# Kernel optimization log

Hardware: AMD Instinct MI355X
Metric: run time of the kernel (lower is better)

Reference implementation:

```python
import jax, jax.numpy as jnp
import numpy as np

B, N, E = 4, 10000, 160000
IN, OUT, H, ED = 64, 128, 2, 1
SLOPE = 0.2  # GATv2Conv default negative_slope


def _seg_softmax(logits, seg, n):
    # logits: [Ef, H]; softmax over edges sharing the same dst node, per head
    m = jax.ops.segment_max(logits, seg, num_segments=n)
    e = jnp.exp(logits - m[seg])
    d = jax.ops.segment_sum(e, seg, num_segments=n)
    return e / d[seg]


def setup_inputs() -> dict:
    key = jax.random.key(0)
    ks = jax.random.split(key, 10)
    s = 0.05
    return {
        "node_feats": jax.random.normal(ks[0], (B, N, IN), jnp.float32),
        "edge_index": jax.random.randint(ks[1], (2, E), 0, N, dtype=jnp.int64),
        "edge_attr": jax.random.normal(ks[2], (E, ED), jnp.float32),
        "Wl": jax.random.normal(ks[3], (IN, H * OUT), jnp.float32) * s,
        "bl": jax.random.normal(ks[4], (H * OUT,), jnp.float32) * s,
        "Wr": jax.random.normal(ks[5], (IN, H * OUT), jnp.float32) * s,
        "br": jax.random.normal(ks[6], (H * OUT,), jnp.float32) * s,
        "We": jax.random.normal(ks[7], (ED, H * OUT), jnp.float32) * s,
        "att": jax.random.normal(ks[8], (H, OUT), jnp.float32) * s,
        "bias": jax.random.normal(ks[9], (H * OUT,), jnp.float32) * s,
    }


def reference(node_feats, edge_index, edge_attr, Wl, bl, Wr, br, We, att, bias):
    src, dst = edge_index[0], edge_index[1]
    # PyG add_self_loops(fill_value='mean'): self-loop attr = mean of incoming edge attrs per node
    ones = jnp.ones((E,), edge_attr.dtype)
    deg = jax.ops.segment_sum(ones, dst, num_segments=N)
    loop_attr = jax.ops.segment_sum(edge_attr, dst, num_segments=N) / jnp.maximum(deg, 1.0)[:, None]
    sl = jnp.arange(N)
    src_f = jnp.concatenate([src, sl])           # [Ef] with Ef = E + N
    dst_f = jnp.concatenate([dst, sl])
    e_feat = (jnp.concatenate([edge_attr, loop_attr], axis=0) @ We).reshape(-1, H, OUT)  # [Ef,H,C]

    xl = (node_feats @ Wl + bl).reshape(B, N, H, OUT)  # lin_l(x)
    xr = (node_feats @ Wr + br).reshape(B, N, H, OUT)  # lin_r(x)

    # GATv2: score on leaky_relu(x_l[src] + x_r[dst] + lin_edge(e))
    msg = jax.nn.leaky_relu(xl[:, src_f] + xr[:, dst_f] + e_feat[None], SLOPE)  # [B,Ef,H,C]
    logits = jnp.einsum('behc,hc->beh', msg, att)                               # [B,Ef,H]
    alpha = jax.vmap(lambda l: _seg_softmax(l, dst_f, N))(logits)               # [B,Ef,H]

    weighted = alpha[..., None] * xl[:, src_f]                                  # [B,Ef,H,C]
    out = jax.vmap(lambda w: jax.ops.segment_sum(w, dst_f, num_segments=N))(weighted)  # [B,N,H,C]
    return out.reshape(B, N, H * OUT) + bias
```

## Files before the change

### kernel.cpp

```cpp
#include <hip/hip_runtime.h>
#include <hip/hip_bf16.h>

#define BQ 4
#define NN 10000
#define EE 160000
#define HC 256
#define SLOPEK 0.2f
#define CAPE 128

typedef __attribute__((ext_vector_type(8))) short bf16x8;
typedef __attribute__((ext_vector_type(4))) float f32x4;
typedef __attribute__((ext_vector_type(2))) float f32x2;

__device__ __forceinline__ unsigned short f2bf(float f) {
    unsigned int u = __float_as_uint(f);
    u = (u + 0x7FFFu + ((u >> 16) & 1u)) >> 16;
    return (unsigned short)u;
}
__device__ __forceinline__ f32x2 bf2(unsigned int u) {
    return (f32x2){__uint_as_float(u << 16), __uint_as_float(u & 0xFFFF0000u)};
}

__global__ __launch_bounds__(256) void k_wpack(
    const float* __restrict__ Wl, const float* __restrict__ bl,
    const float* __restrict__ Wr, const float* __restrict__ br,
    unsigned short* __restrict__ wp, float* __restrict__ bp,
    int* __restrict__ zbase)
{
    if (blockIdx.x >= 130) {
        const int i = (blockIdx.x - 130) * 256 + threadIdx.x;
        if (i < 2 * NN) zbase[i] = 0;
        return;
    }
    const int tid = blockIdx.x * 256 + threadIdx.x;
    if (tid < 32768) {
        const int j  = tid & 7;
        const int l  = (tid >> 3) & 63;
        const int s  = (tid >> 9) & 1;
        const int ct = tid >> 10;
        const int col = ct * 16 + (l & 15);
        const int kk  = s * 32 + ((l >> 4) << 3) + j;
        const float w = (col < 256) ? Wl[kk * 256 + col] : Wr[kk * 256 + (col - 256)];
        wp[tid] = f2bf(w);
    } else if (tid < 32768 + 512) {
        const int c = tid - 32768;
        bp[c] = (c < 256) ? bl[c] : br[c - 256];
    }
}

__global__ __launch_bounds__(256) void k_pre(
    const float* __restrict__ x, const unsigned short* __restrict__ wp,
    const float* __restrict__ bp,
    unsigned short* __restrict__ xl, unsigned short* __restrict__ xr,
    const int* __restrict__ ei, const float* __restrict__ ea,
    int* __restrict__ cnt, float* __restrict__ asum,
    int2* __restrict__ cmeta)
{
    __shared__ unsigned short st[64][264];

    if (blockIdx.x >= 625) {
        const int e = (blockIdx.x - 625) * 256 + threadIdx.x;
        const int   sn = ei[e];
        const int   d  = ei[EE + e];
        const float a  = ea[e];
        const int pos  = atomicAdd(&cnt[d], 1);
        atomicAdd(&asum[d], a);
        if (pos < CAPE - 1)
            cmeta[d * CAPE + pos] = make_int2(sn << 10, __float_as_int(a));
        return;
    }
    const int t = threadIdx.x;
    const int w = t >> 6, l = t & 63;
    const int row0 = blockIdx.x * 64 + w * 16;
    const int arow = row0 + (l & 15);
    const float* xp = x + (size_t)arow * 64 + ((l >> 4) << 3);

    bf16x8 a[2];
#pragma unroll
    for (int s = 0; s < 2; ++s) {
        const float4 lo = *reinterpret_cast<const float4*>(xp + s * 32);
        const float4 hi = *reinterpret_cast<const float4*>(xp + s * 32 + 4);
        union { bf16x8 v; unsigned short u[8]; } tt;
        tt.u[0] = f2bf(lo.x); tt.u[1] = f2bf(lo.y); tt.u[2] = f2bf(lo.z); tt.u[3] = f2bf(lo.w);
        tt.u[4] = f2bf(hi.x); tt.u[5] = f2bf(hi.y); tt.u[6] = f2bf(hi.z); tt.u[7] = f2bf(hi.w);
        a[s] = tt.v;
    }
    const int colb = l & 15;
    const int rsub = (l >> 4) << 2;

    for (int h = 0; h < 2; ++h) {
        for (int g4 = 0; g4 < 4; ++g4) {
            f32x4 acc[4] = {{0.f,0.f,0.f,0.f},{0.f,0.f,0.f,0.f},
                            {0.f,0.f,0.f,0.f},{0.f,0.f,0.f,0.f}};
#pragma unroll
            for (int c = 0; c < 4; ++c) {
                const int ct = h * 16 + g4 * 4 + c;
                const bf16x8 b0 = *reinterpret_cast<const bf16x8*>(wp + (((ct * 2 + 0) * 64 + l) << 3));
                const bf16x8 b1 = *reinterpret_cast<const bf16x8*>(wp + (((ct * 2 + 1) * 64 + l) << 3));
                acc[c] = __builtin_amdgcn_mfma_f32_16x16x32_bf16(a[0], b0, acc[c], 0, 0, 0);
                acc[c] = __builtin_amdgcn_mfma_f32_16x16x32_bf16(a[1], b1, acc[c], 0, 0, 0);
            }
#pragma unroll
            for (int c = 0; c < 4; ++c) {
                const int colh = (g4 * 4 + c) * 16 + colb;
                const float bv = bp[h * 256 + colh];
#pragma unroll
                for (int r = 0; r < 4; ++r)
                    st[w * 16 + rsub + r][colh] = f2bf(acc[c][r] + bv);
            }
        }
        __syncthreads();
        unsigned short* __restrict__ dstb = h ? xr : xl;
        for (int rr = (t >> 5); rr < 64; rr += 8) {
            const int row = blockIdx.x * 64 + rr;
            const int bb = row / NN;
            const int n = row - bb * NN;
            const uint4 v = *reinterpret_cast<const uint4*>(&st[rr][(t & 31) * 8]);
            *reinterpret_cast<uint4*>(dstb + (((size_t)(n * 4 + bb)) << 8) + (t & 31) * 8) = v;
        }
        __syncthreads();
    }
}

__global__ __launch_bounds__(256) void k_gat(
    const unsigned short* __restrict__ xl, const unsigned short* __restrict__ xr,
    const int* __restrict__ cnt, const float* __restrict__ asum,
    const int2* __restrict__ cmeta,
    const float* __restrict__ We, const float* __restrict__ att,
    const float* __restrict__ bias, float* __restrict__ outp)
{
    const int t  = threadIdx.x;
    const int wv = t >> 6, ln = t & 63;
    const int W  = blockIdx.x * 4 + wv;
    const int n  = W >> 1;
    const int bp = W & 1;
    const int b  = bp * 2 + (ln >> 5);
    const int ch0 = (ln & 31) * 8;

    int dg0 = cnt[n];
    if (dg0 > 63) dg0 = 63;
    const int dg = __builtin_amdgcn_readfirstlane(dg0);
    const int2 md0 = cmeta[n * CAPE + ln];
    int   ms = md0.x;
    float ma = __int_as_float(md0.y);
    if (ln == dg) {
        ms = n << 10;
        ma = asum[n] / fmaxf((float)dg, 1.0f);
    }
    const int ntot = dg + 1;

    f32x2 we2[4], at2[4], xr2[4], acc2[4];
    {
        const float4* Wp = reinterpret_cast<const float4*>(We + ch0);
        const float4* Ap = reinterpret_cast<const float4*>(att + ch0);
#pragma unroll
        for (int j = 0; j < 2; ++j) {
            const float4 w4 = Wp[j], a4 = Ap[j];
            we2[2*j+0] = (f32x2){w4.x, w4.y};
            we2[2*j+1] = (f32x2){w4.z, w4.w};
            at2[2*j+0] = (f32x2){a4.x, a4.y};
            at2[2*j+1] = (f32x2){a4.z, a4.w};
        }
        const uint4 r0 = *reinterpret_cast<const uint4*>(
            xr + ((size_t)n << 10) + (b << 8) + ch0);
        xr2[0] = bf2(r0.x); xr2[1] = bf2(r0.y); xr2[2] = bf2(r0.z); xr2[3] = bf2(r0.w);
    }
    const f32x2 km1 = {SLOPEK - 1.f, SLOPEK - 1.f};
    const f32x2 z2  = {0.f, 0.f};
#pragma unroll
    for (int k = 0; k < 4; ++k) acc2[k] = z2;
    float sh = 0.f;

    const unsigned short* __restrict__ xlp = xl + (b << 8) + ch0;

    uint4 A0, A1, A2, A3, A4, A5, A6, A7;
    float ea0, ea1, ea2, ea3, ea4, ea5, ea6, ea7;

#define LOADSLOT(S, IDX) do { \
        const int ii_ = (IDX); \
        const int ic_ = ii_ < dg ? ii_ : dg; \
        const int   s_ = __builtin_amdgcn_readlane(ms, ic_); \
        ea##S = __int_as_float(__builtin_amdgcn_readlane(__float_as_int(ma), ic_)); \
        A##S = *reinterpret_cast<const uint4*>(xlp + s_); \
    } while (0)

    auto edgeC = [&](const uint4& A, float a0) {
        f32x2 xv2[4];
        xv2[0] = bf2(A.x); xv2[1] = bf2(A.y); xv2[2] = bf2(A.z); xv2[3] = bf2(A.w);

        const f32x2 a02 = {a0, a0};
        f32x2 qa = z2, qb = z2;
#pragma unroll
        for (int j = 0; j < 4; ++j) {
            f32x2 s = xv2[j] + xr2[j];
            f32x2 v = __builtin_elementwise_fma(a02, we2[j], s);
            f32x2 vm = __builtin_elementwise_min(v, z2);
            v = __builtin_elementwise_fma(km1, vm, v);
            if (j & 1) qb = __builtin_elementwise_fma(v, at2[j], qb);
            else       qa = __builtin_elementwise_fma(v, at2[j], qa);
        }
        const f32x2 q2 = qa + qb;
        float p = q2.x + q2.y;
        p += __shfl_xor(p, 1);
        p += __shfl_xor(p, 2);
        p += __shfl_xor(p, 4);
        p += __shfl_xor(p, 8);
        const float e = __expf(p);
        sh += e;
        const f32x2 e2 = {e, e};
#pragma unroll
        for (int j = 0; j < 4; ++j)
            acc2[j] = __builtin_elementwise_fma(e2, xv2[j], acc2[j]);
    };

    LOADSLOT(0, 0); LOADSLOT(1, 1); LOADSLOT(2, 2); LOADSLOT(3, 3);
    LOADSLOT(4, 4); LOADSLOT(5, 5); LOADSLOT(6, 6);

    int i = 0;
    for (; i + 7 < ntot; i += 8) {
        LOADSLOT(7, i + 7);  edgeC(A0, ea0);
        LOADSLOT(0, i + 8);  edgeC(A1, ea1);
        LOADSLOT(1, i + 9);  edgeC(A2, ea2);
        LOADSLOT(2, i + 10); edgeC(A3, ea3);
        LOADSLOT(3, i + 11); edgeC(A4, ea4);
        LOADSLOT(4, i + 12); edgeC(A5, ea5);
        LOADSLOT(5, i + 13); edgeC(A6, ea6);
        LOADSLOT(6, i + 14); edgeC(A7, ea7);
    }
    if (i     < ntot) edgeC(A0, ea0);
    if (i + 1 < ntot) edgeC(A1, ea1);
    if (i + 2 < ntot) edgeC(A2, ea2);
    if (i + 3 < ntot) edgeC(A3, ea3);
    if (i + 4 < ntot) edgeC(A4, ea4);
    if (i + 5 < ntot) edgeC(A5, ea5);
    if (i + 6 < ntot) edgeC(A6, ea6);
#undef LOADSLOT

    const float inv = 1.0f / sh;
    float* ob = outp + (((size_t)(b * NN + n)) << 8) + ch0;
    const float4* Bp = reinterpret_cast<const float4*>(bias + ch0);
#pragma unroll
    for (int j = 0; j < 2; ++j) {
        const float4 b4 = Bp[j];
        float4 o;
        o.x = fmaf(acc2[2*j+0].x, inv, b4.x);
        o.y = fmaf(acc2[2*j+0].y, inv, b4.y);
        o.z = fmaf(acc2[2*j+1].x, inv, b4.z);
        o.w = fmaf(acc2[2*j+1].y, inv, b4.w);
        reinterpret_cast<float4*>(ob)[j] = o;
    }
}

extern "C" void kernel_launch(void* const* d_in, const int* in_sizes, int n_in,
                              void* d_out, int out_size, void* d_ws, size_t ws_size,
                              hipStream_t stream)
{
    (void)in_sizes; (void)n_in; (void)out_size; (void)ws_size;
    const float* x    = (const float*)d_in[0];
    const int*   ei   = (const int*)d_in[1];
    const float* ea   = (const float*)d_in[2];
    const float* Wl   = (const float*)d_in[3];
    const float* bl   = (const float*)d_in[4];
    const float* Wr   = (const float*)d_in[5];
    const float* br   = (const float*)d_in[6];
    const float* We   = (const float*)d_in[7];
    const float* att  = (const float*)d_in[8];
    const float* bias = (const float*)d_in[9];
    float* outp = (float*)d_out;

    const size_t R = (size_t)BQ * NN;
    unsigned short* xl16 = (unsigned short*)d_ws;
    unsigned short* xr16 = xl16 + R * HC;
    int*   cnt   = (int*)(xr16 + R * HC);
    float* asum  = (float*)(cnt + NN);
    int2*  cmeta = (int2*)(asum + NN);
    unsigned short* wp = (unsigned short*)(cmeta + (size_t)NN * CAPE);
    float* bp    = (float*)(wp + 32768);

    k_wpack<<<130 + (2 * NN + 255) / 256, 256, 0, stream>>>(Wl, bl, Wr, br, wp, bp, cnt);
    k_pre  <<<1250, 256, 0, stream>>>(x, wp, bp, xl16, xr16,
                                      ei, ea, cnt, asum, cmeta);
    k_gat  <<<(2 * NN) / 4, 256, 0, stream>>>(xl16, xr16, cnt, asum, cmeta,
                                              We, att, bias, outp);
}
```

Before: 91.21 us.

## Stream gathered xl rows into LDS ring via global_load_lds and split edge kernel

The gather loop in the attention kernel now issues direct global-to-LDS loads into a per-wave 8-slot ring instead of holding eight register-resident uint4 slots, with explicit vmcnt waits to pace consumption. The aim is to cut register pressure and keep a deep gather pipeline in flight. Separately, the linear projection and edge bucketing are split into their own kernels, and counter zeroing moves to a memset. The extra launches add overhead, and the per-edge LDS round-trip plus vmcnt waits could serialize the gather. Each wave loads a full 512-short row covering both batches and reads its own lanes back from LDS.

After: 132.5 us. +45.3%, slower.

```diff
diff --git a/kernel.cpp b/kernel.cpp
--- a/kernel.cpp
+++ b/kernel.cpp
@@ -21,17 +21,18 @@
     return (f32x2){__uint_as_float(u << 16), __uint_as_float(u & 0xFFFF0000u)};
 }
 
+__device__ __forceinline__ void gload_lds16(const unsigned short* g, unsigned short* l) {
+    __builtin_amdgcn_global_load_lds(
+        (const __attribute__((address_space(1))) unsigned int*)g,
+        (__attribute__((address_space(3))) unsigned int*)l,
+        16, 0, 0);
+}
+
 __global__ __launch_bounds__(256) void k_wpack(
     const float* __restrict__ Wl, const float* __restrict__ bl,
     const float* __restrict__ Wr, const float* __restrict__ br,
-    unsigned short* __restrict__ wp, float* __restrict__ bp,
-    int* __restrict__ zbase)
-{
-    if (blockIdx.x >= 130) {
-        const int i = (blockIdx.x - 130) * 256 + threadIdx.x;
-        if (i < 2 * NN) zbase[i] = 0;
-        return;
-    }
+    unsigned short* __restrict__ wp, float* __restrict__ bp)
+{
     const int tid = blockIdx.x * 256 + threadIdx.x;
     if (tid < 32768) {
         const int j  = tid & 7;
@@ -48,27 +49,13 @@
     }
 }
 
-__global__ __launch_bounds__(256) void k_pre(
+__global__ __launch_bounds__(256) void k_lin(
     const float* __restrict__ x, const unsigned short* __restrict__ wp,
     const float* __restrict__ bp,
-    unsigned short* __restrict__ xl, unsigned short* __restrict__ xr,
-    const int* __restrict__ ei, const float* __restrict__ ea,
-    int* __restrict__ cnt, float* __restrict__ asum,
-    int2* __restrict__ cmeta)
+    unsigned short* __restrict__ xl, unsigned short* __restrict__ xr)
 {
     __shared__ unsigned short st[64][264];
 
-    if (blockIdx.x >= 625) {
-        const int e = (blockIdx.x - 625) * 256 + threadIdx.x;
-        const int   sn = ei[e];
-        const int   d  = ei[EE + e];
-        const float a  = ea[e];
-        const int pos  = atomicAdd(&cnt[d], 1);
-        atomicAdd(&asum[d], a);
-        if (pos < CAPE - 1)
-            cmeta[d * CAPE + pos] = make_int2(sn << 10, __float_as_int(a));
-        return;
-    }
     const int t = threadIdx.x;
     const int w = t >> 6, l = t & 63;
     const int row0 = blockIdx.x * 64 + w * 16;
@@ -122,6 +109,21 @@
     }
 }
 
+__global__ __launch_bounds__(256) void k_edges(
+    const int* __restrict__ ei, const float* __restrict__ ea,
+    int* __restrict__ cnt, float* __restrict__ asum,
+    int2* __restrict__ cmeta)
+{
+    const int e = blockIdx.x * 256 + threadIdx.x;
+    const int   sn = ei[e];
+    const int   d  = ei[EE + e];
+    const float a  = ea[e];
+    const int pos  = atomicAdd(&cnt[d], 1);
+    atomicAdd(&asum[d], a);
+    if (pos < CAPE - 1)
+        cmeta[d * CAPE + pos] = make_int2(sn << 10, __float_as_int(a));
+}
+
 __global__ __launch_bounds__(256) void k_gat(
     const unsigned short* __restrict__ xl, const unsigned short* __restrict__ xr,
     const int* __restrict__ cnt, const float* __restrict__ asum,
@@ -129,6 +131,8 @@
     const float* __restrict__ We, const float* __restrict__ att,
     const float* __restrict__ bias, float* __restrict__ outp)
 {
+    __shared__ __align__(16) unsigned short ring[4][8][512];
+
     const int t  = threadIdx.x;
     const int wv = t >> 6, ln = t & 63;
     const int W  = blockIdx.x * 4 + wv;
@@ -171,18 +175,7 @@
     for (int k = 0; k < 4; ++k) acc2[k] = z2;
     float sh = 0.f;
 
-    const unsigned short* __restrict__ xlp = xl + (b << 8) + ch0;
-
-    uint4 A0, A1, A2, A3, A4, A5, A6, A7;
-    float ea0, ea1, ea2, ea3, ea4, ea5, ea6, ea7;
-
-#define LOADSLOT(S, IDX) do { \
-        const int ii_ = (IDX); \
-        const int ic_ = ii_ < dg ? ii_ : dg; \
-        const int   s_ = __builtin_amdgcn_readlane(ms, ic_); \
-        ea##S = __int_as_float(__builtin_amdgcn_readlane(__float_as_int(ma), ic_)); \
-        A##S = *reinterpret_cast<const uint4*>(xlp + s_); \
-    } while (0)
+    const unsigned short* __restrict__ xlp = xl + (bp << 9) + ln * 8;
 
     auto edgeC = [&](const uint4& A, float a0) {
         f32x2 xv2[4];
@@ -213,28 +206,28 @@
             acc2[j] = __builtin_elementwise_fma(e2, xv2[j], acc2[j]);
     };
 
-    LOADSLOT(0, 0); LOADSLOT(1, 1); LOADSLOT(2, 2); LOADSLOT(3, 3);
-    LOADSLOT(4, 4); LOADSLOT(5, 5); LOADSLOT(6, 6);
-
-    int i = 0;
-    for (; i + 7 < ntot; i += 8) {
-        LOADSLOT(7, i + 7);  edgeC(A0, ea0);
-        LOADSLOT(0, i + 8);  edgeC(A1, ea1);
-        LOADSLOT(1, i + 9);  edgeC(A2, ea2);
-        LOADSLOT(2, i + 10); edgeC(A3, ea3);
-        LOADSLOT(3, i + 11); edgeC(A4, ea4);
-        LOADSLOT(4, i + 12); edgeC(A5, ea5);
-        LOADSLOT(5, i + 13); edgeC(A6, ea6);
-        LOADSLOT(6, i + 14); edgeC(A7, ea7);
-    }
-    if (i     < ntot) edgeC(A0, ea0);
-    if (i + 1 < ntot) edgeC(A1, ea1);
-    if (i + 2 < ntot) edgeC(A2, ea2);
-    if (i + 3 < ntot) edgeC(A3, ea3);
-    if (i + 4 < ntot) edgeC(A4, ea4);
-    if (i + 5 < ntot) edgeC(A5, ea5);
-    if (i + 6 < ntot) edgeC(A6, ea6);
-#undef LOADSLOT
+    asm volatile("s_waitcnt vmcnt(0)" ::: "memory");
+
+#pragma unroll
+    for (int k = 0; k < 7; ++k) {
+        const int ic = k < dg ? k : dg;
+        const int s_ = __builtin_amdgcn_readlane(ms, ic);
+        gload_lds16(xlp + s_, &ring[wv][k][0]);
+    }
+
+    for (int i = 0; i < ntot; ++i) {
+        {
+            const int idx = i + 7;
+            const int ic = idx < dg ? idx : dg;
+            const int s_ = __builtin_amdgcn_readlane(ms, ic);
+            gload_lds16(xlp + s_, &ring[wv][(i + 7) & 7][0]);
+        }
+        asm volatile("s_waitcnt vmcnt(7)" ::: "memory");
+        const uint4 A = *reinterpret_cast<const uint4*>(&ring[wv][i & 7][ln * 8]);
+        const float a0 = __int_as_float(__builtin_amdgcn_readlane(__float_as_int(ma), i));
+        edgeC(A, a0);
+    }
+    asm volatile("s_waitcnt vmcnt(0)" ::: "memory");
 
     const float inv = 1.0f / sh;
     float* ob = outp + (((size_t)(b * NN + n)) << 8) + ch0;
@@ -277,9 +270,11 @@
     unsigned short* wp = (unsigned short*)(cmeta + (size_t)NN * CAPE);
     float* bp    = (float*)(wp + 32768);
 
-    k_wpack<<<130 + (2 * NN + 255) / 256, 256, 0, stream>>>(Wl, bl, Wr, br, wp, bp, cnt);
-    k_pre  <<<1250, 256, 0, stream>>>(x, wp, bp, xl16, xr16,
-                                      ei, ea, cnt, asum, cmeta);
+    hipMemsetAsync(cnt, 0, sizeof(int) * NN * 2, stream);
+
+    k_wpack<<<130, 256, 0, stream>>>(Wl, bl, Wr, br, wp, bp);
+    k_lin  <<<625, 256, 0, stream>>>(x, wp, bp, xl16, xr16);
+    k_edges<<<625, 256, 0, stream>>>(ei, ea, cnt, asum, cmeta);
     k_gat  <<<(2 * NN) / 4, 256, 0, stream>>>(xl16, xr16, cnt, asum, cmeta,
                                               We, att, bias, outp);
 }
```

## Restructure GAT kernel to batch-major layout with packed bf16 edge metadata

Applied to the files above, without the earlier changes.

Stores xl/xr in plain batch-major row order instead of node-interleaved order. Each k_gat block now handles one batch for four nodes, with a full wave covering one node's 256 channels at 4 channels per lane. Edge metadata is packed into a single int (source index in the high 16 bits, bf16 edge attribute in the low 16 bits), halving cmeta traffic. The intent is to cut per-lane register use and metadata bandwidth and to improve batch locality in the xl gathers. The trade-offs are smaller 8-byte gathers, an extra shuffle step per edge, a shallower prefetch pipeline, reduced precision on the edge attribute, and node indices limited to 16 bits.

New measurement: 97.09 us. 6.5% more time.

```diff
diff --git a/kernel.cpp b/kernel.cpp
--- a/kernel.cpp
+++ b/kernel.cpp
@@ -54,7 +54,7 @@
     unsigned short* __restrict__ xl, unsigned short* __restrict__ xr,
     const int* __restrict__ ei, const float* __restrict__ ea,
     int* __restrict__ cnt, float* __restrict__ asum,
-    int2* __restrict__ cmeta)
+    int* __restrict__ cmeta)
 {
     __shared__ unsigned short st[64][264];
 
@@ -66,7 +66,7 @@
         const int pos  = atomicAdd(&cnt[d], 1);
         atomicAdd(&asum[d], a);
         if (pos < CAPE - 1)
-            cmeta[d * CAPE + pos] = make_int2(sn << 10, __float_as_int(a));
+            cmeta[d * CAPE + pos] = (sn << 16) | (int)f2bf(a);
         return;
     }
     const int t = threadIdx.x;
@@ -112,11 +112,9 @@
         __syncthreads();
         unsigned short* __restrict__ dstb = h ? xr : xl;
         for (int rr = (t >> 5); rr < 64; rr += 8) {
-            const int row = blockIdx.x * 64 + rr;
-            const int bb = row / NN;
-            const int n = row - bb * NN;
+            const size_t row = blockIdx.x * 64 + rr;
             const uint4 v = *reinterpret_cast<const uint4*>(&st[rr][(t & 31) * 8]);
-            *reinterpret_cast<uint4*>(dstb + (((size_t)(n * 4 + bb)) << 8) + (t & 31) * 8) = v;
+            *reinterpret_cast<uint4*>(dstb + (row << 8) + (t & 31) * 8) = v;
         }
         __syncthreads();
     }
@@ -125,130 +123,103 @@
 __global__ __launch_bounds__(256) void k_gat(
     const unsigned short* __restrict__ xl, const unsigned short* __restrict__ xr,
     const int* __restrict__ cnt, const float* __restrict__ asum,
-    const int2* __restrict__ cmeta,
+    const int* __restrict__ cmeta,
     const float* __restrict__ We, const float* __restrict__ att,
     const float* __restrict__ bias, float* __restrict__ outp)
 {
     const int t  = threadIdx.x;
     const int wv = t >> 6, ln = t & 63;
-    const int W  = blockIdx.x * 4 + wv;
-    const int n  = W >> 1;
-    const int bp = W & 1;
-    const int b  = bp * 2 + (ln >> 5);
-    const int ch0 = (ln & 31) * 8;
+    const int batch = blockIdx.x & 3;
+    const int n  = (blockIdx.x >> 2) * 4 + wv;
+    const int ch0 = ln * 4;
 
     int dg0 = cnt[n];
     if (dg0 > 63) dg0 = 63;
     const int dg = __builtin_amdgcn_readfirstlane(dg0);
-    const int2 md0 = cmeta[n * CAPE + ln];
-    int   ms = md0.x;
-    float ma = __int_as_float(md0.y);
-    if (ln == dg) {
-        ms = n << 10;
-        ma = asum[n] / fmaxf((float)dg, 1.0f);
-    }
+    int mp = cmeta[n * CAPE + ln];
+    if (ln == dg)
+        mp = (n << 16) | (int)f2bf(asum[n] / fmaxf((float)dg, 1.0f));
     const int ntot = dg + 1;
 
-    f32x2 we2[4], at2[4], xr2[4], acc2[4];
+    f32x2 we2[2], at2[2], xr2[2], acc2[2];
     {
-        const float4* Wp = reinterpret_cast<const float4*>(We + ch0);
-        const float4* Ap = reinterpret_cast<const float4*>(att + ch0);
-#pragma unroll
-        for (int j = 0; j < 2; ++j) {
-            const float4 w4 = Wp[j], a4 = Ap[j];
-            we2[2*j+0] = (f32x2){w4.x, w4.y};
-            we2[2*j+1] = (f32x2){w4.z, w4.w};
-            at2[2*j+0] = (f32x2){a4.x, a4.y};
-            at2[2*j+1] = (f32x2){a4.z, a4.w};
-        }
-        const uint4 r0 = *reinterpret_cast<const uint4*>(
-            xr + ((size_t)n << 10) + (b << 8) + ch0);
-        xr2[0] = bf2(r0.x); xr2[1] = bf2(r0.y); xr2[2] = bf2(r0.z); xr2[3] = bf2(r0.w);
+        const float4 w4 = *reinterpret_cast<const float4*>(We + ch0);
+        const float4 a4 = *reinterpret_cast<const float4*>(att + ch0);
+        we2[0] = (f32x2){w4.x, w4.y}; we2[1] = (f32x2){w4.z, w4.w};
+        at2[0] = (f32x2){a4.x, a4.y}; at2[1] = (f32x2){a4.z, a4.w};
+        const uint2 r0 = *reinterpret_cast<const uint2*>(
+            xr + (((size_t)(batch * NN + n)) << 8) + ch0);
+        xr2[0] = bf2(r0.x); xr2[1] = bf2(r0.y);
     }
     const f32x2 km1 = {SLOPEK - 1.f, SLOPEK - 1.f};
     const f32x2 z2  = {0.f, 0.f};
-#pragma unroll
-    for (int k = 0; k < 4; ++k) acc2[k] = z2;
+    acc2[0] = z2; acc2[1] = z2;
     float sh = 0.f;
 
-    const unsigned short* __restrict__ xlp = xl + (b << 8) + ch0;
-
-    uint4 A0, A1, A2, A3, A4, A5, A6, A7;
-    float ea0, ea1, ea2, ea3, ea4, ea5, ea6, ea7;
+    const unsigned short* __restrict__ xlb = xl + (((size_t)batch * NN) << 8) + ch0;
+
+    uint2 A0, A1, A2, A3;
+    float ea0, ea1, ea2, ea3;
 
 #define LOADSLOT(S, IDX) do { \
         const int ii_ = (IDX); \
         const int ic_ = ii_ < dg ? ii_ : dg; \
-        const int   s_ = __builtin_amdgcn_readlane(ms, ic_); \
-        ea##S = __int_as_float(__builtin_amdgcn_readlane(__float_as_int(ma), ic_)); \
-        A##S = *reinterpret_cast<const uint4*>(xlp + s_); \
+        const int sc_ = __builtin_amdgcn_readlane(mp, ic_); \
+        ea##S = __uint_as_float(((unsigned int)sc_) << 16); \
+        A##S = *reinterpret_cast<const uint2*>(xlb + ((size_t)(sc_ >> 16) << 8)); \
     } while (0)
 
-    auto edgeC = [&](const uint4& A, float a0) {
-        f32x2 xv2[4];
-        xv2[0] = bf2(A.x); xv2[1] = bf2(A.y); xv2[2] = bf2(A.z); xv2[3] = bf2(A.w);
+    auto edgeC = [&](const uint2& A, float a0) {
+        f32x2 xv2[2];
+        xv2[0] = bf2(A.x); xv2[1] = bf2(A.y);
 
         const f32x2 a02 = {a0, a0};
-        f32x2 qa = z2, qb = z2;
-#pragma unroll
-        for (int j = 0; j < 4; ++j) {
+        f32x2 q2 = z2;
+#pragma unroll
+        for (int j = 0; j < 2; ++j) {
             f32x2 s = xv2[j] + xr2[j];
             f32x2 v = __builtin_elementwise_fma(a02, we2[j], s);
             f32x2 vm = __builtin_elementwise_min(v, z2);
             v = __builtin_elementwise_fma(km1, vm, v);
-            if (j & 1) qb = __builtin_elementwise_fma(v, at2[j], qb);
-            else       qa = __builtin_elementwise_fma(v, at2[j], qa);
+            q2 = __builtin_elementwise_fma(v, at2[j], q2);
         }
-        const f32x2 q2 = qa + qb;
         float p = q2.x + q2.y;
         p += __shfl_xor(p, 1);
         p += __shfl_xor(p, 2);
         p += __shfl_xor(p, 4);
         p += __shfl_xor(p, 8);
+        p += __shfl_xor(p, 16);
         const float e = __expf(p);
         sh += e;
         const f32x2 e2 = {e, e};
-#pragma unroll
-        for (int j = 0; j < 4; ++j)
-            acc2[j] = __builtin_elementwise_fma(e2, xv2[j], acc2[j]);
+        acc2[0] = __builtin_elementwise_fma(e2, xv2[0], acc2[0]);
+        acc2[1] = __builtin_elementwise_fma(e2, xv2[1], acc2[1]);
     };
 
-    LOADSLOT(0, 0); LOADSLOT(1, 1); LOADSLOT(2, 2); LOADSLOT(3, 3);
-    LOADSLOT(4, 4); LOADSLOT(5, 5); LOADSLOT(6, 6);
+    LOADSLOT(0, 0);
+    LOADSLOT(1, 1);
+    LOADSLOT(2, 2);
 
     int i = 0;
-    for (; i + 7 < ntot; i += 8) {
-        LOADSLOT(7, i + 7);  edgeC(A0, ea0);
-        LOADSLOT(0, i + 8);  edgeC(A1, ea1);
-        LOADSLOT(1, i + 9);  edgeC(A2, ea2);
-        LOADSLOT(2, i + 10); edgeC(A3, ea3);
-        LOADSLOT(3, i + 11); edgeC(A4, ea4);
-        LOADSLOT(4, i + 12); edgeC(A5, ea5);
-        LOADSLOT(5, i + 13); edgeC(A6, ea6);
-        LOADSLOT(6, i + 14); edgeC(A7, ea7);
+    for (; i + 3 < ntot; i += 4) {
+        LOADSLOT(3, i + 3); edgeC(A0, ea0);
+        LOADSLOT(0, i + 4); edgeC(A1, ea1);
+        LOADSLOT(1, i + 5); edgeC(A2, ea2);
+        LOADSLOT(2, i + 6); edgeC(A3, ea3);
     }
     if (i     < ntot) edgeC(A0, ea0);
     if (i + 1 < ntot) edgeC(A1, ea1);
     if (i + 2 < ntot) edgeC(A2, ea2);
-    if (i + 3 < ntot) edgeC(A3, ea3);
-    if (i + 4 < ntot) edgeC(A4, ea4);
-    if (i + 5 < ntot) edgeC(A5, ea5);
-    if (i + 6 < ntot) edgeC(A6, ea6);
 #undef LOADSLOT
 
     const float inv = 1.0f / sh;
-    float* ob = outp + (((size_t)(b * NN + n)) << 8) + ch0;
-    const float4* Bp = reinterpret_cast<const float4*>(bias + ch0);
-#pragma unroll
-    for (int j = 0; j < 2; ++j) {
-        const float4 b4 = Bp[j];
-        float4 o;
-        o.x = fmaf(acc2[2*j+0].x, inv, b4.x);
-        o.y = fmaf(acc2[2*j+0].y, inv, b4.y);
-        o.z = fmaf(acc2[2*j+1].x, inv, b4.z);
-        o.w = fmaf(acc2[2*j+1].y, inv, b4.w);
-        reinterpret_cast<float4*>(ob)[j] = o;
-    }
+    const float4 b4 = *reinterpret_cast<const float4*>(bias + ch0);
+    float4 o;
+    o.x = fmaf(acc2[0].x, inv, b4.x);
+    o.y = fmaf(acc2[0].y, inv, b4.y);
+    o.z = fmaf(acc2[1].x, inv, b4.z);
+    o.w = fmaf(acc2[1].y, inv, b4.w);
+    *reinterpret_cast<float4*>(outp + (((size_t)(batch * NN + n)) << 8) + ch0) = o;
 }
 
 extern "C" void kernel_launch(void* const* d_in, const int* in_sizes, int n_in,
@@ -273,13 +244,13 @@
     unsigned short* xr16 = xl16 + R * HC;
     int*   cnt   = (int*)(xr16 + R * HC);
     float* asum  = (float*)(cnt + NN);
-    int2*  cmeta = (int2*)(asum + NN);
+    int*   cmeta = (int*)(asum + NN);
     unsigned short* wp = (unsigned short*)(cmeta + (size_t)NN * CAPE);
     float* bp    = (float*)(wp + 32768);
 
     k_wpack<<<130 + (2 * NN + 255) / 256, 256, 0, stream>>>(Wl, bl, Wr, br, wp, bp, cnt);
     k_pre  <<<1250, 256, 0, stream>>>(x, wp, bp, xl16, xr16,
                                       ei, ea, cnt, asum, cmeta);
-    k_gat  <<<(2 * NN) / 4, 256, 0, stream>>>(xl16, xr16, cnt, asum, cmeta,
-                                              We, att, bias, outp);
-}
+    k_gat  <<<NN, 256, 0, stream>>>(xl16, xr16, cnt, asum, cmeta,
+                                    We, att, bias, outp);
+}
```
